# Performance work log

Measured on AMD Instinct MI355X. Metric: run time of the kernel, lower is better.

The kernel has to match this reference:

```python
import jax, jax.numpy as jnp
import numpy as np

B, S, E, HEAD = 8, 2048, 512, 64  # head_size = embeddings_dims // no_of_heads = 512 // 8


def setup_inputs() -> dict:
    key = jax.random.key(0)
    kx, kq, kk, kv, kl = jax.random.split(key, 5)
    x = jax.random.normal(kx, (B, S, E), dtype=jnp.float32)
    # Linear(512 -> 64, bias=False); store as [E, HEAD] so y = x @ W
    Wq = jax.random.normal(kq, (E, HEAD), dtype=jnp.float32) * (E ** -0.5)
    Wk = jax.random.normal(kk, (E, HEAD), dtype=jnp.float32) * (E ** -0.5)
    Wv = jax.random.normal(kv, (E, HEAD), dtype=jnp.float32) * (E ** -0.5)
    # Realistic padding mask: 1 for first `length` tokens, 0 after.
    lengths = jax.random.randint(kl, (B,), S // 2, S + 1)
    mask = (jnp.arange(S)[None, :] < lengths[:, None]).astype(jnp.int32)
    return {"x": x, "Wq": Wq, "Wk": Wk, "Wv": Wv, "mask": mask}


def reference(x, Wq, Wk, Wv, mask):
    # q, k, v: [B, S, HEAD]
    q = x @ Wq
    k = x @ Wk
    v = x @ Wv
    # scores: [B, S, S], scaled by head_size**-0.5 (k.shape[-1] in the original)
    scores = jnp.einsum('bqd,bkd->bqk', q, k) * (HEAD ** -0.5)
    causal = jnp.tril(jnp.ones((S, S), dtype=bool))            # [S, S]
    keep = (mask[:, None, :] != 0) & causal[None, :, :]        # padding mask broadcast over query rows, then causal
    scores = jnp.where(keep, scores, -jnp.inf)
    attn = jax.nn.softmax(scores, axis=-1)                     # [B, S, S]
    out = attn @ v                                             # [B, S, HEAD]
    return out
```

## Files before the change

### kernel.cpp

```cpp
#include <hip/hip_runtime.h>

#define BB 8
#define SS 2048
#define EE 512
#define HD 64
#define CHUNK 256
#define KT 64
#define NCH 8
#define PST 72
#define TST 72
#define XRS 40
#define XKB 640
#define NITEMS 576

typedef __attribute__((ext_vector_type(8))) short bf16x8;
typedef __attribute__((ext_vector_type(4))) float f32x4;

static __device__ __forceinline__ unsigned short f2bf(float f) {
    unsigned u = __builtin_bit_cast(unsigned, f);
    u = (u + 0x7fffu + ((u >> 16) & 1u)) >> 16;
    return (unsigned short)u;
}
static __device__ __forceinline__ unsigned short f2bf_trunc(float f) {
    return (unsigned short)(__builtin_bit_cast(unsigned, f) >> 16);
}
static __device__ __forceinline__ float bf2f(unsigned short h) {
    unsigned u = ((unsigned)h) << 16;
    return __builtin_bit_cast(float, u);
}

__global__ __launch_bounds__(256) void pack_w_kernel(
    const float* __restrict__ Wq, const float* __restrict__ Wk, const float* __restrict__ Wv,
    unsigned short* __restrict__ Wt, int* __restrict__ tickets) {
    if (blockIdx.x == 0 && threadIdx.x == 0) atomicExch(tickets, 0);
    int tid = blockIdx.x * 256 + threadIdx.x;
    if (tid >= 3 * EE * HD) return;
    int w_idx = tid / (EE * HD);
    int rem = tid % (EE * HD);
    int kk = rem / HD, n = rem % HD;
    const float* Wsrc = (w_idx == 0) ? Wq : ((w_idx == 1) ? Wk : Wv);
    float val = Wsrc[kk * HD + n];
    if (w_idx == 0) val *= 0.125f;
    int kb = kk >> 5, kr = kk & 31, quad = kr >> 3, j = kr & 7;
    int t = n >> 4, c = n & 15;
    int lane = quad * 16 + c;
    Wt[w_idx * (EE * HD) + ((kb * 4 + t) * 64 + lane) * 8 + j] = f2bf(val);
}

__global__ __launch_bounds__(256) void qkv_kernel(
    const float* __restrict__ x,
    const unsigned short* __restrict__ Wt,
    unsigned short* __restrict__ q,
    unsigned short* __restrict__ k,
    unsigned short* __restrict__ vT) {
    __shared__ __align__(16) unsigned short Xs[16 * XKB];
    const int tid = threadIdx.x;
    const int lane = tid & 63;
    const int t = tid >> 6;
    const int c = lane & 15, quad = lane >> 4;
    const int r0 = blockIdx.x * 16;

    const float* xt = x + (size_t)r0 * EE;
#pragma unroll
    for (int i = 0; i < 8; ++i) {
        int fi = i * 256 + tid;
        int e4 = fi * 4;
        float4 v4 = *(const float4*)(xt + e4);
        int row = e4 >> 9, col = e4 & 511;
        int kb = col >> 5, cc = col & 31;
        ushort4 pk;
        pk.x = f2bf(v4.x); pk.y = f2bf(v4.y); pk.z = f2bf(v4.z); pk.w = f2bf(v4.w);
        *(ushort4*)(&Xs[kb * XKB + row * XRS + cc]) = pk;
    }
    __syncthreads();

    f32x4 acc[3];
    for (int m = 0; m < 3; ++m) acc[m] = (f32x4){0.f, 0.f, 0.f, 0.f};

    const unsigned short* wbase0 = Wt + t * 512 + lane * 8;
#pragma unroll
    for (int kb = 0; kb < EE / 32; ++kb) {
        bf16x8 afrag = *(const bf16x8*)(&Xs[kb * XKB + c * XRS + quad * 8]);
        const unsigned short* wb = wbase0 + kb * 2048;
#pragma unroll
        for (int m = 0; m < 3; ++m) {
            bf16x8 bfrag = *(const bf16x8*)(wb + m * (EE * HD));
            acc[m] = __builtin_amdgcn_mfma_f32_16x16x32_bf16(afrag, bfrag, acc[m], 0, 0, 0);
        }
    }

    const int col = t * 16 + c;
    for (int r = 0; r < 4; ++r) {
        int row = r0 + quad * 4 + r;
        q[(size_t)row * HD + col] = f2bf(acc[0][r]);
        k[(size_t)row * HD + col] = f2bf(acc[1][r]);
    }
    {
        int row = r0 + quad * 4;
        int b_ = row >> 11, sb = row & (SS - 1);
        ushort4 pk;
        pk.x = f2bf(acc[2][0]); pk.y = f2bf(acc[2][1]);
        pk.z = f2bf(acc[2][2]); pk.w = f2bf(acc[2][3]);
        *(ushort4*)(vT + ((size_t)b_ * HD + col) * SS + sb) = pk;
    }
}

__global__ __launch_bounds__(256, 3) void attn_kernel(
    const unsigned short* __restrict__ q,
    const unsigned short* __restrict__ k,
    const unsigned short* __restrict__ vT,
    const int* __restrict__ mask,
    unsigned short* __restrict__ po,
    float* __restrict__ pl,
    int* __restrict__ tickets,
    float* __restrict__ out) {
    __shared__ __align__(16) unsigned short Ks[2][64 * TST];
    __shared__ __align__(16) unsigned short Vs[2][64 * TST];
    __shared__ __align__(16) unsigned short Ps[4][16 * PST];
    __shared__ int tkt;
    const int tid = threadIdx.x;
    const int lane = tid & 63, wave = tid >> 6;
    const int c = lane & 15, quad = lane >> 4;

    for (;;) {
        __syncthreads();
        if (tid == 0) tkt = atomicAdd(tickets, 1);
        __syncthreads();
        int t = tkt;
        if (t >= NITEMS) break;
        t = NITEMS - 1 - t;
        const int b_ = t / 72;
        int r = t % 72;
        int g = 0;
        while ((g + 1) * (g + 2) <= r) ++g;
        int rr = r - g * (g + 1);
        const int Q = 2 * g + rr / (g + 1);
        const int cx = rr % (g + 1);
        const int kstart = cx * CHUNK;
        const int kend = min(kstart + CHUNK, Q * 128 + 128);
        const int ntiles = (kend - kstart) >> 6;
        const int nch_active = Q / 2 + 1;
        const int r0 = Q * 128 + wave * 32;

        const unsigned short* qb_p = q + (size_t)b_ * SS * HD;
        const unsigned short* kb_p = k + (size_t)b_ * SS * HD;
        const unsigned short* vb = vT + (size_t)b_ * HD * SS;
        const int* mb = mask + b_ * SS;

        bf16x8 aq[2][2];
#pragma unroll
        for (int rt = 0; rt < 2; ++rt) {
            const unsigned short* qrow = qb_p + (size_t)(r0 + rt * 16 + c) * HD + quad * 8;
            aq[rt][0] = *(const bf16x8*)(qrow);
            aq[rt][1] = *(const bf16x8*)(qrow + 32);
        }

        f32x4 o[2][4];
        float l_i[2][4];
#pragma unroll
        for (int rt = 0; rt < 2; ++rt)
            for (int tt = 0; tt < 4; ++tt) {
                o[rt][tt] = (f32x4){0.f, 0.f, 0.f, 0.f};
                l_i[rt][tt] = 0.f;
            }

        auto stage = [&](int buf, int k0) {
            const unsigned short* ksrc = kb_p + (size_t)k0 * HD;
            unsigned short* kd = &Ks[buf][0];
            unsigned short* vd = &Vs[buf][0];
#pragma unroll
            for (int rnd = 0; rnd < 2; ++rnd) {
                int e = (rnd * 256 + tid) * 8;
                int krow = e >> 6, kcol = e & 63;
                *(bf16x8*)(kd + krow * TST + kcol) = *(const bf16x8*)(ksrc + e);
                int t8 = rnd * 256 + tid;
                int vr = t8 >> 3, vc = (t8 & 7) * 8;
                *(bf16x8*)(vd + vr * TST + vc) = *(const bf16x8*)(vb + (size_t)vr * SS + k0 + vc);
            }
        };

        stage(0, kstart);
        for (int kt = 0; kt < ntiles; ++kt) {
            __syncthreads();
            const unsigned short* ks = &Ks[kt & 1][0];
            const unsigned short* vs = &Vs[kt & 1][0];
            const int k0 = kstart + kt * KT;
            bf16x8 kf[4][2];
#pragma unroll
            for (int kg = 0; kg < 4; ++kg) {
                kf[kg][0] = *(const bf16x8*)(ks + (kg * 16 + c) * TST + quad * 8);
                kf[kg][1] = *(const bf16x8*)(ks + (kg * 16 + c) * TST + 32 + quad * 8);
            }
            if (kt + 1 < ntiles) stage((kt + 1) & 1, k0 + KT);
#pragma unroll
            for (int rt = 0; rt < 2; ++rt) {
                const int rbase = r0 + rt * 16;
                const bool fullc = (k0 + KT <= rbase);
                float p[4][4];
#pragma unroll
                for (int kg = 0; kg < 4; ++kg) {
                    f32x4 accs = (f32x4){0.f, 0.f, 0.f, 0.f};
                    accs = __builtin_amdgcn_mfma_f32_16x16x32_bf16(aq[rt][0], kf[kg][0], accs, 0, 0, 0);
                    accs = __builtin_amdgcn_mfma_f32_16x16x32_bf16(aq[rt][1], kf[kg][1], accs, 0, 0, 0);
                    int key = k0 + kg * 16 + c;
                    bool mk = (mb[key] != 0);
                    for (int rr2 = 0; rr2 < 4; ++rr2) {
                        int row = rbase + quad * 4 + rr2;
                        bool keep = mk && (fullc || key <= row);
                        float e = __expf(fminf(accs[rr2], 80.f));
                        float pe = keep ? e : 0.f;
                        p[kg][rr2] = pe;
                        l_i[rt][rr2] += pe;
                    }
                }
                unsigned short* pbuf = &Ps[wave][0];
#pragma unroll
                for (int kg = 0; kg < 4; ++kg)
                    for (int rr2 = 0; rr2 < 4; ++rr2)
                        pbuf[(quad * 4 + rr2) * PST + kg * 16 + c] = f2bf_trunc(p[kg][rr2]);
                bf16x8 pa0 = *(const bf16x8*)(pbuf + c * PST + quad * 8);
                bf16x8 pa1 = *(const bf16x8*)(pbuf + c * PST + 32 + quad * 8);
#pragma unroll
                for (int tt = 0; tt < 4; ++tt) {
                    bf16x8 bv0 = *(const bf16x8*)(vs + (tt * 16 + c) * TST + quad * 8);
                    bf16x8 bv1 = *(const bf16x8*)(vs + (tt * 16 + c) * TST + 32 + quad * 8);
                    o[rt][tt] = __builtin_amdgcn_mfma_f32_16x16x32_bf16(pa0, bv0, o[rt][tt], 0, 0, 0);
                    o[rt][tt] = __builtin_amdgcn_mfma_f32_16x16x32_bf16(pa1, bv1, o[rt][tt], 0, 0, 0);
                }
            }
        }

#pragma unroll
        for (int rt = 0; rt < 2; ++rt)
            for (int rr2 = 0; rr2 < 4; ++rr2) {
                float s = l_i[rt][rr2];
                s += __shfl_xor(s, 1);
                s += __shfl_xor(s, 2);
                s += __shfl_xor(s, 4);
                s += __shfl_xor(s, 8);
                l_i[rt][rr2] = s;
            }

        if (nch_active == 1) {
#pragma unroll
            for (int rt = 0; rt < 2; ++rt)
                for (int rr2 = 0; rr2 < 4; ++rr2) {
                    int row = r0 + rt * 16 + quad * 4 + rr2;
                    float l = l_i[rt][rr2];
                    float inv = (l > 0.f) ? 1.f / l : 0.f;
                    for (int tt = 0; tt < 4; ++tt)
                        out[((size_t)b_ * SS + row) * HD + tt * 16 + c] = o[rt][tt][rr2] * inv;
                }
            continue;
        }

#pragma unroll
        for (int rt = 0; rt < 2; ++rt)
            for (int rr2 = 0; rr2 < 4; ++rr2) {
                int row_abs = r0 + rt * 16 + quad * 4 + rr2;
                int qb_i = row_abs >> 6, rl = row_abs & 63;
                size_t base = (size_t)(b_ * 32 + qb_i) * NCH + cx;
                float l = l_i[rt][rr2];
                float inv = (l > 0.f) ? 1.f / l : 0.f;
                for (int tt = 0; tt < 4; ++tt)
                    po[base * 4096 + (size_t)rl * 64 + tt * 16 + c] = f2bf(o[rt][tt][rr2] * inv);
                if (c == 0) pl[base * 64 + rl] = l;
            }
    }
}

__global__ __launch_bounds__(256) void combine_kernel(
    const unsigned short* __restrict__ po,
    const float* __restrict__ pl,
    float* __restrict__ out) {
    int t = blockIdx.x * 256 + threadIdx.x;
    if (t >= BB * (SS - 256) * HD) return;
    int d = t & 63;
    int rg = t >> 6;
    int b_ = rg / (SS - 256);
    int row = 256 + rg % (SS - 256);
    int qb = row >> 6, rl = row & 63;
    int nch = row / CHUNK + 1;
    size_t base = (size_t)(b_ * 32 + qb) * NCH;
    float L = 0.f, acc = 0.f;
    for (int c = 0; c < nch; ++c) {
        float l = pl[(base + c) * 64 + rl];
        L += l;
        acc += l * bf2f(po[(base + c) * 4096 + (size_t)rl * 64 + d]);
    }
    out[((size_t)b_ * SS + row) * HD + d] = (L > 0.f) ? acc / L : 0.f;
}

extern "C" void kernel_launch(void* const* d_in, const int* in_sizes, int n_in,
                              void* d_out, int out_size, void* d_ws, size_t ws_size,
                              hipStream_t stream) {
    const float* x = (const float*)d_in[0];
    const float* Wq = (const float*)d_in[1];
    const float* Wk = (const float*)d_in[2];
    const float* Wv = (const float*)d_in[3];
    const int* mask = (const int*)d_in[4];
    float* out = (float*)d_out;

    unsigned short* ws = (unsigned short*)d_ws;
    unsigned short* Wt = ws;
    unsigned short* q = Wt + 3 * EE * HD;
    unsigned short* kk = q + (size_t)BB * SS * HD;
    unsigned short* vT = kk + (size_t)BB * SS * HD;
    unsigned short* po = vT + (size_t)BB * SS * HD;
    float* pl = (float*)(po + (size_t)BB * 32 * NCH * 4096);
    int* tickets = (int*)(pl + (size_t)BB * 32 * NCH * 64);

    pack_w_kernel<<<dim3((3 * EE * HD + 255) / 256), dim3(256), 0, stream>>>(Wq, Wk, Wv, Wt, tickets);
    qkv_kernel<<<dim3(BB * SS / 16), dim3(256), 0, stream>>>(x, Wt, q, kk, vT);
    attn_kernel<<<dim3(768), dim3(256), 0, stream>>>(q, kk, vT, mask, po, pl, tickets, out);
    combine_kernel<<<dim3((BB * (SS - 256) * HD + 255) / 256), dim3(256), 0, stream>>>(po, pl, out);
}
```

Before: 124.5 us.

## Replace atomic ticket scheduler with static block mapping and double QKV rows per block

The attention kernel drops its persistent atomic-ticket work queue and launches one block per work item, mapping blockIdx directly to items in reverse order so the longest items start first. This removes the per-item atomic and the two barriers around it, at the cost of relying on the hardware block scheduler for load balance. The QKV projection kernel now processes 32 rows per block instead of 16, reusing each loaded weight fragment for two row tiles. That halves the weight reads per row but doubles shared memory per block and halves the block count.

```diff
diff --git a/kernel.cpp b/kernel.cpp
--- a/kernel.cpp
+++ b/kernel.cpp
@@ -10,7 +10,7 @@
 #define PST 72
 #define TST 72
 #define XRS 40
-#define XKB 640
+#define XKB 1280
 #define NITEMS 576
 
 typedef __attribute__((ext_vector_type(8))) short bf16x8;
@@ -31,8 +31,7 @@
 
 __global__ __launch_bounds__(256) void pack_w_kernel(
     const float* __restrict__ Wq, const float* __restrict__ Wk, const float* __restrict__ Wv,
-    unsigned short* __restrict__ Wt, int* __restrict__ tickets) {
-    if (blockIdx.x == 0 && threadIdx.x == 0) atomicExch(tickets, 0);
+    unsigned short* __restrict__ Wt) {
     int tid = blockIdx.x * 256 + threadIdx.x;
     if (tid >= 3 * EE * HD) return;
     int w_idx = tid / (EE * HD);
@@ -58,11 +57,11 @@
     const int lane = tid & 63;
     const int t = tid >> 6;
     const int c = lane & 15, quad = lane >> 4;
-    const int r0 = blockIdx.x * 16;
+    const int r0 = blockIdx.x * 32;
 
     const float* xt = x + (size_t)r0 * EE;
 #pragma unroll
-    for (int i = 0; i < 8; ++i) {
+    for (int i = 0; i < 16; ++i) {
         int fi = i * 256 + tid;
         int e4 = fi * 4;
         float4 v4 = *(const float4*)(xt + e4);
@@ -74,33 +73,41 @@
     }
     __syncthreads();
 
-    f32x4 acc[3];
-    for (int m = 0; m < 3; ++m) acc[m] = (f32x4){0.f, 0.f, 0.f, 0.f};
+    f32x4 acc[2][3];
+#pragma unroll
+    for (int rt = 0; rt < 2; ++rt)
+        for (int m = 0; m < 3; ++m) acc[rt][m] = (f32x4){0.f, 0.f, 0.f, 0.f};
 
     const unsigned short* wbase0 = Wt + t * 512 + lane * 8;
 #pragma unroll
     for (int kb = 0; kb < EE / 32; ++kb) {
-        bf16x8 afrag = *(const bf16x8*)(&Xs[kb * XKB + c * XRS + quad * 8]);
         const unsigned short* wb = wbase0 + kb * 2048;
-#pragma unroll
-        for (int m = 0; m < 3; ++m) {
-            bf16x8 bfrag = *(const bf16x8*)(wb + m * (EE * HD));
-            acc[m] = __builtin_amdgcn_mfma_f32_16x16x32_bf16(afrag, bfrag, acc[m], 0, 0, 0);
+        bf16x8 bfrag[3];
+#pragma unroll
+        for (int m = 0; m < 3; ++m) bfrag[m] = *(const bf16x8*)(wb + m * (EE * HD));
+#pragma unroll
+        for (int rt = 0; rt < 2; ++rt) {
+            bf16x8 afrag = *(const bf16x8*)(&Xs[kb * XKB + (rt * 16 + c) * XRS + quad * 8]);
+#pragma unroll
+            for (int m = 0; m < 3; ++m)
+                acc[rt][m] = __builtin_amdgcn_mfma_f32_16x16x32_bf16(afrag, bfrag[m], acc[rt][m], 0, 0, 0);
         }
     }
 
     const int col = t * 16 + c;
-    for (int r = 0; r < 4; ++r) {
-        int row = r0 + quad * 4 + r;
-        q[(size_t)row * HD + col] = f2bf(acc[0][r]);
-        k[(size_t)row * HD + col] = f2bf(acc[1][r]);
-    }
-    {
-        int row = r0 + quad * 4;
+#pragma unroll
+    for (int rt = 0; rt < 2; ++rt) {
+        const int rb = r0 + rt * 16;
+        for (int r = 0; r < 4; ++r) {
+            int row = rb + quad * 4 + r;
+            q[(size_t)row * HD + col] = f2bf(acc[rt][0][r]);
+            k[(size_t)row * HD + col] = f2bf(acc[rt][1][r]);
+        }
+        int row = rb + quad * 4;
         int b_ = row >> 11, sb = row & (SS - 1);
         ushort4 pk;
-        pk.x = f2bf(acc[2][0]); pk.y = f2bf(acc[2][1]);
-        pk.z = f2bf(acc[2][2]); pk.w = f2bf(acc[2][3]);
+        pk.x = f2bf(acc[rt][2][0]); pk.y = f2bf(acc[rt][2][1]);
+        pk.z = f2bf(acc[rt][2][2]); pk.w = f2bf(acc[rt][2][3]);
         *(ushort4*)(vT + ((size_t)b_ * HD + col) * SS + sb) = pk;
     }
 }
@@ -112,161 +119,152 @@
     const int* __restrict__ mask,
     unsigned short* __restrict__ po,
     float* __restrict__ pl,
-    int* __restrict__ tickets,
     float* __restrict__ out) {
     __shared__ __align__(16) unsigned short Ks[2][64 * TST];
     __shared__ __align__(16) unsigned short Vs[2][64 * TST];
     __shared__ __align__(16) unsigned short Ps[4][16 * PST];
-    __shared__ int tkt;
     const int tid = threadIdx.x;
     const int lane = tid & 63, wave = tid >> 6;
     const int c = lane & 15, quad = lane >> 4;
 
-    for (;;) {
+    int t = NITEMS - 1 - blockIdx.x;
+    const int b_ = t / 72;
+    int r = t % 72;
+    int g = 0;
+    while ((g + 1) * (g + 2) <= r) ++g;
+    int rr = r - g * (g + 1);
+    const int Q = 2 * g + rr / (g + 1);
+    const int cx = rr % (g + 1);
+    const int kstart = cx * CHUNK;
+    const int kend = min(kstart + CHUNK, Q * 128 + 128);
+    const int ntiles = (kend - kstart) >> 6;
+    const int nch_active = Q / 2 + 1;
+    const int r0 = Q * 128 + wave * 32;
+
+    const unsigned short* qb_p = q + (size_t)b_ * SS * HD;
+    const unsigned short* kb_p = k + (size_t)b_ * SS * HD;
+    const unsigned short* vb = vT + (size_t)b_ * HD * SS;
+    const int* mb = mask + b_ * SS;
+
+    bf16x8 aq[2][2];
+#pragma unroll
+    for (int rt = 0; rt < 2; ++rt) {
+        const unsigned short* qrow = qb_p + (size_t)(r0 + rt * 16 + c) * HD + quad * 8;
+        aq[rt][0] = *(const bf16x8*)(qrow);
+        aq[rt][1] = *(const bf16x8*)(qrow + 32);
+    }
+
+    f32x4 o[2][4];
+    float l_i[2][4];
+#pragma unroll
+    for (int rt = 0; rt < 2; ++rt)
+        for (int tt = 0; tt < 4; ++tt) {
+            o[rt][tt] = (f32x4){0.f, 0.f, 0.f, 0.f};
+            l_i[rt][tt] = 0.f;
+        }
+
+    auto stage = [&](int buf, int k0) {
+        const unsigned short* ksrc = kb_p + (size_t)k0 * HD;
+        unsigned short* kd = &Ks[buf][0];
+        unsigned short* vd = &Vs[buf][0];
+#pragma unroll
+        for (int rnd = 0; rnd < 2; ++rnd) {
+            int e = (rnd * 256 + tid) * 8;
+            int krow = e >> 6, kcol = e & 63;
+            *(bf16x8*)(kd + krow * TST + kcol) = *(const bf16x8*)(ksrc + e);
+            int t8 = rnd * 256 + tid;
+            int vr = t8 >> 3, vc = (t8 & 7) * 8;
+            *(bf16x8*)(vd + vr * TST + vc) = *(const bf16x8*)(vb + (size_t)vr * SS + k0 + vc);
+        }
+    };
+
+    stage(0, kstart);
+    for (int kt = 0; kt < ntiles; ++kt) {
         __syncthreads();
-        if (tid == 0) tkt = atomicAdd(tickets, 1);
-        __syncthreads();
-        int t = tkt;
-        if (t >= NITEMS) break;
-        t = NITEMS - 1 - t;
-        const int b_ = t / 72;
-        int r = t % 72;
-        int g = 0;
-        while ((g + 1) * (g + 2) <= r) ++g;
-        int rr = r - g * (g + 1);
-        const int Q = 2 * g + rr / (g + 1);
-        const int cx = rr % (g + 1);
-        const int kstart = cx * CHUNK;
-        const int kend = min(kstart + CHUNK, Q * 128 + 128);
-        const int ntiles = (kend - kstart) >> 6;
-        const int nch_active = Q / 2 + 1;
-        const int r0 = Q * 128 + wave * 32;
-
-        const unsigned short* qb_p = q + (size_t)b_ * SS * HD;
-        const unsigned short* kb_p = k + (size_t)b_ * SS * HD;
-        const unsigned short* vb = vT + (size_t)b_ * HD * SS;
-        const int* mb = mask + b_ * SS;
-
-        bf16x8 aq[2][2];
+        const unsigned short* ks = &Ks[kt & 1][0];
+        const unsigned short* vs = &Vs[kt & 1][0];
+        const int k0 = kstart + kt * KT;
+        bf16x8 kf[4][2];
+#pragma unroll
+        for (int kg = 0; kg < 4; ++kg) {
+            kf[kg][0] = *(const bf16x8*)(ks + (kg * 16 + c) * TST + quad * 8);
+            kf[kg][1] = *(const bf16x8*)(ks + (kg * 16 + c) * TST + 32 + quad * 8);
+        }
+        if (kt + 1 < ntiles) stage((kt + 1) & 1, k0 + KT);
 #pragma unroll
         for (int rt = 0; rt < 2; ++rt) {
-            const unsigned short* qrow = qb_p + (size_t)(r0 + rt * 16 + c) * HD + quad * 8;
-            aq[rt][0] = *(const bf16x8*)(qrow);
-            aq[rt][1] = *(const bf16x8*)(qrow + 32);
-        }
-
-        f32x4 o[2][4];
-        float l_i[2][4];
-#pragma unroll
-        for (int rt = 0; rt < 2; ++rt)
-            for (int tt = 0; tt < 4; ++tt) {
-                o[rt][tt] = (f32x4){0.f, 0.f, 0.f, 0.f};
-                l_i[rt][tt] = 0.f;
-            }
-
-        auto stage = [&](int buf, int k0) {
-            const unsigned short* ksrc = kb_p + (size_t)k0 * HD;
-            unsigned short* kd = &Ks[buf][0];
-            unsigned short* vd = &Vs[buf][0];
-#pragma unroll
-            for (int rnd = 0; rnd < 2; ++rnd) {
-                int e = (rnd * 256 + tid) * 8;
-                int krow = e >> 6, kcol = e & 63;
-                *(bf16x8*)(kd + krow * TST + kcol) = *(const bf16x8*)(ksrc + e);
-                int t8 = rnd * 256 + tid;
-                int vr = t8 >> 3, vc = (t8 & 7) * 8;
-                *(bf16x8*)(vd + vr * TST + vc) = *(const bf16x8*)(vb + (size_t)vr * SS + k0 + vc);
-            }
-        };
-
-        stage(0, kstart);
-        for (int kt = 0; kt < ntiles; ++kt) {
-            __syncthreads();
-            const unsigned short* ks = &Ks[kt & 1][0];
-            const unsigned short* vs = &Vs[kt & 1][0];
-            const int k0 = kstart + kt * KT;
-            bf16x8 kf[4][2];
+            const int rbase = r0 + rt * 16;
+            const bool fullc = (k0 + KT <= rbase);
+            float p[4][4];
 #pragma unroll
             for (int kg = 0; kg < 4; ++kg) {
-                kf[kg][0] = *(const bf16x8*)(ks + (kg * 16 + c) * TST + quad * 8);
-                kf[kg][1] = *(const bf16x8*)(ks + (kg * 16 + c) * TST + 32 + quad * 8);
-            }
-            if (kt + 1 < ntiles) stage((kt + 1) & 1, k0 + KT);
-#pragma unroll
-            for (int rt = 0; rt < 2; ++rt) {
-                const int rbase = r0 + rt * 16;
-                const bool fullc = (k0 + KT <= rbase);
-                float p[4][4];
-#pragma unroll
-                for (int kg = 0; kg < 4; ++kg) {
-                    f32x4 accs = (f32x4){0.f, 0.f, 0.f, 0.f};
-                    accs = __builtin_amdgcn_mfma_f32_16x16x32_bf16(aq[rt][0], kf[kg][0], accs, 0, 0, 0);
-                    accs = __builtin_amdgcn_mfma_f32_16x16x32_bf16(aq[rt][1], kf[kg][1], accs, 0, 0, 0);
-                    int key = k0 + kg * 16 + c;
-                    bool mk = (mb[key] != 0);
-                    for (int rr2 = 0; rr2 < 4; ++rr2) {
-                        int row = rbase + quad * 4 + rr2;
-                        bool keep = mk && (fullc || key <= row);
-                        float e = __expf(fminf(accs[rr2], 80.f));
-                        float pe = keep ? e : 0.f;
-                        p[kg][rr2] = pe;
-                        l_i[rt][rr2] += pe;
-                    }
-                }
-                unsigned short* pbuf = &Ps[wave][0];
-#pragma unroll
-                for (int kg = 0; kg < 4; ++kg)
-                    for (int rr2 = 0; rr2 < 4; ++rr2)
-                        pbuf[(quad * 4 + rr2) * PST + kg * 16 + c] = f2bf_trunc(p[kg][rr2]);
-                bf16x8 pa0 = *(const bf16x8*)(pbuf + c * PST + quad * 8);
-                bf16x8 pa1 = *(const bf16x8*)(pbuf + c * PST + 32 + quad * 8);
-#pragma unroll
-                for (int tt = 0; tt < 4; ++tt) {
-                    bf16x8 bv0 = *(const bf16x8*)(vs + (tt * 16 + c) * TST + quad * 8);
-                    bf16x8 bv1 = *(const bf16x8*)(vs + (tt * 16 + c) * TST + 32 + quad * 8);
-                    o[rt][tt] = __builtin_amdgcn_mfma_f32_16x16x32_bf16(pa0, bv0, o[rt][tt], 0, 0, 0);
-                    o[rt][tt] = __builtin_amdgcn_mfma_f32_16x16x32_bf16(pa1, bv1, o[rt][tt], 0, 0, 0);
+                f32x4 accs = (f32x4){0.f, 0.f, 0.f, 0.f};
+                accs = __builtin_amdgcn_mfma_f32_16x16x32_bf16(aq[rt][0], kf[kg][0], accs, 0, 0, 0);
+                accs = __builtin_amdgcn_mfma_f32_16x16x32_bf16(aq[rt][1], kf[kg][1], accs, 0, 0, 0);
+                int key = k0 + kg * 16 + c;
+                bool mk = (mb[key] != 0);
+                for (int rr2 = 0; rr2 < 4; ++rr2) {
+                    int row = rbase + quad * 4 + rr2;
+                    bool keep = mk && (fullc || key <= row);
+                    float e = __expf(fminf(accs[rr2], 80.f));
+                    float pe = keep ? e : 0.f;
+                    p[kg][rr2] = pe;
+                    l_i[rt][rr2] += pe;
                 }
             }
-        }
-
+            unsigned short* pbuf = &Ps[wave][0];
+#pragma unroll
+            for (int kg = 0; kg < 4; ++kg)
+                for (int rr2 = 0; rr2 < 4; ++rr2)
+                    pbuf[(quad * 4 + rr2) * PST + kg * 16 + c] = f2bf_trunc(p[kg][rr2]);
+            bf16x8 pa0 = *(const bf16x8*)(pbuf + c * PST + quad * 8);
+            bf16x8 pa1 = *(const bf16x8*)(pbuf + c * PST + 32 + quad * 8);
+#pragma unroll
+            for (int tt = 0; tt < 4; ++tt) {
+                bf16x8 bv0 = *(const bf16x8*)(vs + (tt * 16 + c) * TST + quad * 8);
+                bf16x8 bv1 = *(const bf16x8*)(vs + (tt * 16 + c) * TST + 32 + quad * 8);
+                o[rt][tt] = __builtin_amdgcn_mfma_f32_16x16x32_bf16(pa0, bv0, o[rt][tt], 0, 0, 0);
+                o[rt][tt] = __builtin_amdgcn_mfma_f32_16x16x32_bf16(pa1, bv1, o[rt][tt], 0, 0, 0);
+            }
+        }
+    }
+
+#pragma unroll
+    for (int rt = 0; rt < 2; ++rt)
+        for (int rr2 = 0; rr2 < 4; ++rr2) {
+            float s = l_i[rt][rr2];
+            s += __shfl_xor(s, 1);
+            s += __shfl_xor(s, 2);
+            s += __shfl_xor(s, 4);
+            s += __shfl_xor(s, 8);
+            l_i[rt][rr2] = s;
+        }
+
+    if (nch_active == 1) {
 #pragma unroll
         for (int rt = 0; rt < 2; ++rt)
             for (int rr2 = 0; rr2 < 4; ++rr2) {
-                float s = l_i[rt][rr2];
-                s += __shfl_xor(s, 1);
-                s += __shfl_xor(s, 2);
-                s += __shfl_xor(s, 4);
-                s += __shfl_xor(s, 8);
-                l_i[rt][rr2] = s;
-            }
-
-        if (nch_active == 1) {
-#pragma unroll
-            for (int rt = 0; rt < 2; ++rt)
-                for (int rr2 = 0; rr2 < 4; ++rr2) {
-                    int row = r0 + rt * 16 + quad * 4 + rr2;
-                    float l = l_i[rt][rr2];
-                    float inv = (l > 0.f) ? 1.f / l : 0.f;
-                    for (int tt = 0; tt < 4; ++tt)
-                        out[((size_t)b_ * SS + row) * HD + tt * 16 + c] = o[rt][tt][rr2] * inv;
-                }
-            continue;
-        }
-
-#pragma unroll
-        for (int rt = 0; rt < 2; ++rt)
-            for (int rr2 = 0; rr2 < 4; ++rr2) {
-                int row_abs = r0 + rt * 16 + quad * 4 + rr2;
-                int qb_i = row_abs >> 6, rl = row_abs & 63;
-                size_t base = (size_t)(b_ * 32 + qb_i) * NCH + cx;
+                int row = r0 + rt * 16 + quad * 4 + rr2;
                 float l = l_i[rt][rr2];
                 float inv = (l > 0.f) ? 1.f / l : 0.f;
                 for (int tt = 0; tt < 4; ++tt)
-                    po[base * 4096 + (size_t)rl * 64 + tt * 16 + c] = f2bf(o[rt][tt][rr2] * inv);
-                if (c == 0) pl[base * 64 + rl] = l;
+                    out[((size_t)b_ * SS + row) * HD + tt * 16 + c] = o[rt][tt][rr2] * inv;
             }
-    }
+        return;
+    }
+
+#pragma unroll
+    for (int rt = 0; rt < 2; ++rt)
+        for (int rr2 = 0; rr2 < 4; ++rr2) {
+            int row_abs = r0 + rt * 16 + quad * 4 + rr2;
+            int qb_i = row_abs >> 6, rl = row_abs & 63;
+            size_t base = (size_t)(b_ * 32 + qb_i) * NCH + cx;
+            float l = l_i[rt][rr2];
+            float inv = (l > 0.f) ? 1.f / l : 0.f;
+            for (int tt = 0; tt < 4; ++tt)
+                po[base * 4096 + (size_t)rl * 64 + tt * 16 + c] = f2bf(o[rt][tt][rr2] * inv);
+            if (c == 0) pl[base * 64 + rl] = l;
+        }
 }
 
 __global__ __launch_bounds__(256) void combine_kernel(
@@ -308,10 +306,9 @@
     unsigned short* vT = kk + (size_t)BB * SS * HD;
     unsigned short* po = vT + (size_t)BB * SS * HD;
     float* pl = (float*)(po + (size_t)BB * 32 * NCH * 4096);
-    int* tickets = (int*)(pl + (size_t)BB * 32 * NCH * 64);
-
-    pack_w_kernel<<<dim3((3 * EE * HD + 255) / 256), dim3(256), 0, stream>>>(Wq, Wk, Wv, Wt, tickets);
-    qkv_kernel<<<dim3(BB * SS / 16), dim3(256), 0, stream>>>(x, Wt, q, kk, vT);
-    attn_kernel<<<dim3(768), dim3(256), 0, stream>>>(q, kk, vT, mask, po, pl, tickets, out);
+
+    pack_w_kernel<<<dim3((3 * EE * HD + 255) / 256), dim3(256), 0, stream>>>(Wq, Wk, Wv, Wt);
+    qkv_kernel<<<dim3(BB * SS / 32), dim3(256), 0, stream>>>(x, Wt, q, kk, vT);
+    attn_kernel<<<dim3(NITEMS), dim3(256), 0, stream>>>(q, kk, vT, mask, po, pl, out);
     combine_kernel<<<dim3((BB * (SS - 256) * HD + 255) / 256), dim3(256), 0, stream>>>(po, pl, out);
 }
```

Measured after the change: 113.7 us. 1.1x faster.
